# Kernel tuning notes

Hardware: AMD Instinct MI355X
Metric: run time of the kernel (lower is better)

The kernel has to match this reference:

```python
import jax, jax.numpy as jnp
import numpy as np

B, IN, E, H, V, T = 512, 256, 256, 512, 32000, 32


def setup_inputs() -> dict:
    key = jax.random.key(0)
    ks = jax.random.split(key, 8)
    s = 0.05
    return {
        "x": jax.random.normal(ks[0], (B, IN), jnp.float32),
        "agent_w": jax.random.normal(ks[1], (H, IN), jnp.float32) * s,
        "agent_b": jnp.zeros((H,), jnp.float32),
        "sos": jax.random.normal(ks[2], (E,), jnp.float32) * 0.01,
        "emb": jax.random.normal(ks[3], (V, E), jnp.float32) * s,
        "W_ih": jax.random.normal(ks[4], (3 * H, E), jnp.float32) * s,
        "W_hh": jax.random.normal(ks[5], (3 * H, H), jnp.float32) * s,
        "b_ih": jnp.zeros((3 * H,), jnp.float32),
        "b_hh": jnp.zeros((3 * H,), jnp.float32),
        "W_out": jax.random.normal(ks[6], (V, H), jnp.float32) * s,
        "b_out": jnp.zeros((V,), jnp.float32),
        "W_stop": jax.random.normal(ks[7], (1, H), jnp.float32) * s,
        "b_stop": jnp.zeros((1,), jnp.float32),
    }


def _gru_cell(inp, h, W_ih, W_hh, b_ih, b_hh):
    gi = inp @ W_ih.T + b_ih              # [B, 3H]
    gh = h @ W_hh.T + b_hh                # [B, 3H]
    i_r, i_z, i_n = jnp.split(gi, 3, axis=1)
    h_r, h_z, h_n = jnp.split(gh, 3, axis=1)
    r = jax.nn.sigmoid(i_r + h_r)
    z = jax.nn.sigmoid(i_z + h_z)
    n = jnp.tanh(i_n + r * h_n)
    return (1.0 - z) * n + z * h


def reference(x, agent_w, agent_b, sos, emb, W_ih, W_hh, b_ih, b_hh,
              W_out, b_out, W_stop, b_stop):
    h0 = x @ agent_w.T + agent_b                       # agent(x) -> [B, H]
    inp0 = jnp.broadcast_to(sos, (x.shape[0], sos.shape[0]))
    keys = jax.random.split(jax.random.key(42), T)

    def step(carry, k):
        h, inp = carry
        h = _gru_cell(inp, h, W_ih, W_hh, b_ih, b_hh)  # noise_scale=0 -> no noise
        symb_logits = h @ W_out.T + b_out              # [B, V]
        stop_logit = (h @ W_stop.T + b_stop)[:, 0]     # [B]
        logp = jax.nn.log_softmax(symb_logits, axis=1)
        k1, k2 = jax.random.split(k)
        symb = jax.random.categorical(k1, symb_logits, axis=1)          # [B] int
        p_stop = jax.nn.sigmoid(stop_logit)
        stop = jax.random.bernoulli(k2, p_stop).astype(jnp.float32)     # [B]
        symb_lp = jnp.take_along_axis(logp, symb[:, None], axis=1)[:, 0]
        # Bernoulli: log p = s - softplus(s), log(1-p) = -softplus(s)
        sp = jax.nn.softplus(stop_logit)
        stop_lp = stop * stop_logit - sp
        symb_ent = -jnp.sum(jnp.exp(logp) * logp, axis=1)
        stop_ent = sp - stop_logit * p_stop
        inp_next = emb[symb]
        return (h, inp_next), (symb, stop, symb_lp, stop_lp, symb_ent, stop_ent)

    _, ys = jax.lax.scan(step, (h0, inp0), keys)
    symb_seq, stop_seq, symb_lp, stop_lp, symb_ent, stop_ent = ys
    # [T, B] -> [B, T]
    tr = lambda a: a.T
    return (tr(symb_seq), tr(stop_seq).astype(jnp.int32),
            tr(symb_lp), tr(stop_lp), tr(symb_ent), tr(stop_ent))
```

## Files before the change

### kernel.cpp

```cpp
#include <hip/hip_runtime.h>
#include <hip/hip_bf16.h>
#include <stdint.h>

#define JAX_PARTITIONABLE 1

#define Bz 512
#define INz 256
#define Ez 256
#define Hz 512
#define Vz 32000
#define Tz 32
#define BTz (Bz * Tz)
#define TINYF 1.17549435e-38f

typedef float otype;
__device__ __forceinline__ void store_out(otype* out, int idx, float v) {
  out[idx] = v;
}

__device__ __forceinline__ uint32_t rotl32(uint32_t x, int r) {
  return (x << r) | (x >> (32 - r));
}
__device__ __forceinline__ void threefry2x32(uint32_t k0, uint32_t k1,
                                             uint32_t x0, uint32_t x1,
                                             uint32_t& o0, uint32_t& o1) {
  const uint32_t ks2 = k0 ^ k1 ^ 0x1BD11BDAu;
  x0 += k0; x1 += k1;
#define TF_R4(a, b, c, d)                              \
  x0 += x1; x1 = rotl32(x1, a); x1 ^= x0;              \
  x0 += x1; x1 = rotl32(x1, b); x1 ^= x0;              \
  x0 += x1; x1 = rotl32(x1, c); x1 ^= x0;              \
  x0 += x1; x1 = rotl32(x1, d); x1 ^= x0;
  TF_R4(13, 15, 26, 6)  x0 += k1;  x1 += ks2 + 1u;
  TF_R4(17, 29, 16, 24) x0 += ks2; x1 += k0 + 2u;
  TF_R4(13, 15, 26, 6)  x0 += k0;  x1 += k1 + 3u;
  TF_R4(17, 29, 16, 24) x0 += k1;  x1 += ks2 + 4u;
  TF_R4(13, 15, 26, 6)  x0 += ks2; x1 += k0 + 5u;
#undef TF_R4
  o0 = x0; o1 = x1;
}
__device__ __forceinline__ uint32_t rand_bits32(uint32_t ka, uint32_t kb,
                                                uint32_t idx, uint32_t n) {
#if JAX_PARTITIONABLE
  (void)n;
  uint32_t o0, o1;
  threefry2x32(ka, kb, 0u, idx, o0, o1);
  return o0 ^ o1;
#else
  uint32_t half = n >> 1;
  uint32_t o0, o1;
  if (idx < half) { threefry2x32(ka, kb, idx, idx + half, o0, o1); return o0; }
  threefry2x32(ka, kb, idx - half, idx, o0, o1); return o1;
#endif
}
__device__ __forceinline__ float bits_to_f01(uint32_t bits) {
  return __uint_as_float((bits >> 9) | 0x3f800000u) - 1.0f;
}

__global__ void RnnSenderReinforce_36799279792759_kernel(otype* __restrict__ out,
                                                         int n, float v) {
  int i = blockIdx.x * 256 + threadIdx.x;
  if (i < n) out[i] = v;
}

__global__ void keys_kernel(uint32_t* __restrict__ keys) {
  int t = threadIdx.x;
  if (t >= Tz) return;
  uint32_t ka, kb;
#if JAX_PARTITIONABLE
  threefry2x32(0u, 42u, 0u, (uint32_t)t, ka, kb);
#else
  {
    uint32_t j0 = 2u * t, j1 = 2u * t + 1u;
    uint32_t a0, a1, b0, b1;
    if (j0 < Tz) { threefry2x32(0u, 42u, j0, j0 + Tz, a0, a1); ka = a0; }
    else         { threefry2x32(0u, 42u, j0 - Tz, j0, a0, a1); ka = a1; }
    if (j1 < Tz) { threefry2x32(0u, 42u, j1, j1 + Tz, b0, b1); kb = b0; }
    else         { threefry2x32(0u, 42u, j1 - Tz, j1, b0, b1); kb = b1; }
  }
#endif
  uint32_t o0, o1;
#if JAX_PARTITIONABLE
  threefry2x32(ka, kb, 0u, 0u, o0, o1);
  keys[t * 4 + 0] = o0; keys[t * 4 + 1] = o1;
  threefry2x32(ka, kb, 0u, 1u, o0, o1);
  keys[t * 4 + 2] = o0; keys[t * 4 + 3] = o1;
#else
  uint32_t p0, p1, q0, q1;
  threefry2x32(ka, kb, 0u, 2u, p0, p1);
  threefry2x32(ka, kb, 1u, 3u, q0, q1);
  keys[t * 4 + 0] = p0; keys[t * 4 + 1] = q0;
  keys[t * 4 + 2] = p1; keys[t * 4 + 3] = q1;
#endif
}

#define GBM 64
#define GBN 64
#define GBK 32
#define LDSS 68

__device__ __forceinline__ void gemm_bt_body(const float* __restrict__ A,
                                             const float* __restrict__ W,
                                             const float* __restrict__ bias,
                                             float* __restrict__ C,
                                             int M, int N, int K,
                                             int bx, int by,
                                             float* As, float* Bs) {
  const int tid = threadIdx.x;
  const int tx = tid & 15;
  const int ty = tid >> 4;
  const int m0 = by * GBM;
  const int n0 = bx * GBN;
  const int lr = tid >> 3;
  const int lc = (tid & 7) << 2;

  float acc[4][4] = {};
  const float* Ap = A + (size_t)(m0 + lr) * K + lc;
  const float* Wp = W + (size_t)(n0 + lr) * K + lc;
  const size_t rstep = (size_t)32 * K;

  for (int k0 = 0; k0 < K; k0 += GBK) {
    float4 a0 = *(const float4*)(Ap + k0);
    float4 a1 = *(const float4*)(Ap + k0 + rstep);
    float4 b0 = *(const float4*)(Wp + k0);
    float4 b1 = *(const float4*)(Wp + k0 + rstep);
    __syncthreads();
    As[(lc + 0) * LDSS + lr] = a0.x;
    As[(lc + 1) * LDSS + lr] = a0.y;
    As[(lc + 2) * LDSS + lr] = a0.z;
    As[(lc + 3) * LDSS + lr] = a0.w;
    As[(lc + 0) * LDSS + lr + 32] = a1.x;
    As[(lc + 1) * LDSS + lr + 32] = a1.y;
    As[(lc + 2) * LDSS + lr + 32] = a1.z;
    As[(lc + 3) * LDSS + lr + 32] = a1.w;
    Bs[(lc + 0) * LDSS + lr] = b0.x;
    Bs[(lc + 1) * LDSS + lr] = b0.y;
    Bs[(lc + 2) * LDSS + lr] = b0.z;
    Bs[(lc + 3) * LDSS + lr] = b0.w;
    Bs[(lc + 0) * LDSS + lr + 32] = b1.x;
    Bs[(lc + 1) * LDSS + lr + 32] = b1.y;
    Bs[(lc + 2) * LDSS + lr + 32] = b1.z;
    Bs[(lc + 3) * LDSS + lr + 32] = b1.w;
    __syncthreads();
#pragma unroll
    for (int kk = 0; kk < GBK; kk++) {
      float4 af = *(const float4*)&As[kk * LDSS + (ty << 2)];
      float4 bf = *(const float4*)&Bs[kk * LDSS + (tx << 2)];
      float ar[4] = {af.x, af.y, af.z, af.w};
      float br[4] = {bf.x, bf.y, bf.z, bf.w};
#pragma unroll
      for (int i = 0; i < 4; i++)
#pragma unroll
        for (int j = 0; j < 4; j++)
          acc[i][j] = fmaf(ar[i], br[j], acc[i][j]);
    }
  }

  const int nc = n0 + (tx << 2);
  float4 bv;
  bv.x = bias[nc + 0]; bv.y = bias[nc + 1]; bv.z = bias[nc + 2]; bv.w = bias[nc + 3];
#pragma unroll
  for (int i = 0; i < 4; i++) {
    int m = m0 + (ty << 2) + i;
    float4 o;
    o.x = acc[i][0] + bv.x;
    o.y = acc[i][1] + bv.y;
    o.z = acc[i][2] + bv.z;
    o.w = acc[i][3] + bv.w;
    *(float4*)(C + (size_t)m * N + nc) = o;
  }
}

__global__ __launch_bounds__(256) void gemm_bt(const float* __restrict__ A,
                                               const float* __restrict__ W,
                                               const float* __restrict__ bias,
                                               float* __restrict__ C,
                                               int M, int N, int K) {
  __shared__ __align__(16) float As[GBK * LDSS];
  __shared__ __align__(16) float Bs[GBK * LDSS];
  gemm_bt_body(A, W, bias, C, M, N, K, blockIdx.x, blockIdx.y, As, Bs);
}

__global__ __launch_bounds__(256) void gru2_kernel(const float* __restrict__ inp,
                                                   const float* __restrict__ Wih,
                                                   const float* __restrict__ bih,
                                                   float* __restrict__ gi,
                                                   const float* __restrict__ h,
                                                   const float* __restrict__ Whh,
                                                   const float* __restrict__ bhh,
                                                   float* __restrict__ gh) {
  __shared__ __align__(16) float As[GBK * LDSS];
  __shared__ __align__(16) float Bs[GBK * LDSS];
  if (blockIdx.z == 0)
    gemm_bt_body(inp, Wih, bih, gi, Bz, 3 * Hz, Ez, blockIdx.x, blockIdx.y, As, Bs);
  else
    gemm_bt_body(h, Whh, bhh, gh, Bz, 3 * Hz, Hz, blockIdx.x, blockIdx.y, As, Bs);
}

#define QBM 256
#define QBN 128
#define QBK 32
#define QLDA 260
#define QLDB 132

__global__ __launch_bounds__(512, 4) void gemm256_bt(const float* __restrict__ A,
                                                     const float* __restrict__ W,
                                                     const float* __restrict__ bias,
                                                     float* __restrict__ C,
                                                     int M, int N, int K) {
  __shared__ __align__(16) float As[QBK * QLDA];
  __shared__ __align__(16) float Bs[QBK * QLDB];
  const int tid = threadIdx.x;
  const int tx = tid & 15;
  const int ty = tid >> 4;

  const int nP = N / QBN;
  const int G = nP >> 3;
  const int lim = G << 4;
  int b = blockIdx.x;
  int P, mi;
  if (b < lim) {
    int g = b >> 4, r = b & 15;
    mi = r >> 3;
    P = (g << 3) + (r & 7);
  } else {
    int e = b - lim;
    P = (G << 3) + (e & 1);
    mi = e >> 1;
  }
  const int m0 = mi * QBM;
  const int n0 = P * QBN;

  const int ar = tid >> 1;
  const int ak = (tid & 1) << 4;
  const int br = tid >> 2;
  const int bk = (tid & 3) << 2;

  const float* Ap = A + (size_t)(m0 + ar) * K + ak;
  const float* Wp = W + (size_t)(n0 + br) * K + bk;

  float4 a0 = *(const float4*)(Ap);
  float4 a1 = *(const float4*)(Ap + 4);
  float4 a2 = *(const float4*)(Ap + 8);
  float4 a3 = *(const float4*)(Ap + 12);
  float4 b0 = *(const float4*)(Wp);
  float4 b1 = *(const float4*)(Wp + 16);

  float acc[8][8] = {};

  for (int k0 = 0; k0 < K; k0 += QBK) {
    __syncthreads();
    As[(ak + 0) * QLDA + ar] = a0.x;
    As[(ak + 1) * QLDA + ar] = a0.y;
    As[(ak + 2) * QLDA + ar] = a0.z;
    As[(ak + 3) * QLDA + ar] = a0.w;
    As[(ak + 4) * QLDA + ar] = a1.x;
    As[(ak + 5) * QLDA + ar] = a1.y;
    As[(ak + 6) * QLDA + ar] = a1.z;
    As[(ak + 7) * QLDA + ar] = a1.w;
    As[(ak + 8) * QLDA + ar] = a2.x;
    As[(ak + 9) * QLDA + ar] = a2.y;
    As[(ak + 10) * QLDA + ar] = a2.z;
    As[(ak + 11) * QLDA + ar] = a2.w;
    As[(ak + 12) * QLDA + ar] = a3.x;
    As[(ak + 13) * QLDA + ar] = a3.y;
    As[(ak + 14) * QLDA + ar] = a3.z;
    As[(ak + 15) * QLDA + ar] = a3.w;
    Bs[(bk + 0) * QLDB + br] = b0.x;
    Bs[(bk + 1) * QLDB + br] = b0.y;
    Bs[(bk + 2) * QLDB + br] = b0.z;
    Bs[(bk + 3) * QLDB + br] = b0.w;
    Bs[(16 + bk + 0) * QLDB + br] = b1.x;
    Bs[(16 + bk + 1) * QLDB + br] = b1.y;
    Bs[(16 + bk + 2) * QLDB + br] = b1.z;
    Bs[(16 + bk + 3) * QLDB + br] = b1.w;
    __syncthreads();
    if (k0 + QBK < K) {
      a0 = *(const float4*)(Ap + k0 + QBK);
      a1 = *(const float4*)(Ap + k0 + QBK + 4);
      a2 = *(const float4*)(Ap + k0 + QBK + 8);
      a3 = *(const float4*)(Ap + k0 + QBK + 12);
      b0 = *(const float4*)(Wp + k0 + QBK);
      b1 = *(const float4*)(Wp + k0 + QBK + 16);
    }
#pragma unroll 4
    for (int kk = 0; kk < QBK; kk++) {
      float4 xa0 = *(const float4*)&As[kk * QLDA + (ty << 2)];
      float4 xa1 = *(const float4*)&As[kk * QLDA + 128 + (ty << 2)];
      float4 xb0 = *(const float4*)&Bs[kk * QLDB + (tx << 2)];
      float4 xb1 = *(const float4*)&Bs[kk * QLDB + 64 + (tx << 2)];
      float ar8[8] = {xa0.x, xa0.y, xa0.z, xa0.w, xa1.x, xa1.y, xa1.z, xa1.w};
      float br8[8] = {xb0.x, xb0.y, xb0.z, xb0.w, xb1.x, xb1.y, xb1.z, xb1.w};
#pragma unroll
      for (int i = 0; i < 8; i++)
#pragma unroll
        for (int j = 0; j < 8; j++)
          acc[i][j] = fmaf(ar8[i], br8[j], acc[i][j]);
    }
  }

  const int nc0 = n0 + (tx << 2);
  const float4 bv0 = *(const float4*)(bias + nc0);
  const float4 bv1 = *(const float4*)(bias + nc0 + 64);
#pragma unroll
  for (int hf = 0; hf < 2; hf++) {
#pragma unroll
    for (int i = 0; i < 4; i++) {
      const int m = m0 + hf * 128 + (ty << 2) + i;
      float* Cp = C + (size_t)m * N + nc0;
      float4 o;
      o.x = acc[hf * 4 + i][0] + bv0.x;
      o.y = acc[hf * 4 + i][1] + bv0.y;
      o.z = acc[hf * 4 + i][2] + bv0.z;
      o.w = acc[hf * 4 + i][3] + bv0.w;
      *(float4*)Cp = o;
      float4 o2;
      o2.x = acc[hf * 4 + i][4] + bv1.x;
      o2.y = acc[hf * 4 + i][5] + bv1.y;
      o2.z = acc[hf * 4 + i][6] + bv1.z;
      o2.w = acc[hf * 4 + i][7] + bv1.w;
      *(float4*)(Cp + 64) = o2;
    }
  }
}

__global__ __launch_bounds__(512) void gates_stop_kernel(
    const float* __restrict__ gi, const float* __restrict__ gh,
    float* __restrict__ h, const float* __restrict__ W_stop,
    const float* __restrict__ b_stop, const uint32_t* __restrict__ keys,
    int t, otype* __restrict__ out) {
  __shared__ float hrow[Hz];
  const int b = blockIdx.x;
  const int j = threadIdx.x;
  const float* gib = gi + (size_t)b * (3 * Hz);
  const float* ghb = gh + (size_t)b * (3 * Hz);
  float ir = gib[j], iz = gib[j + Hz], in_ = gib[j + 2 * Hz];
  float hr = ghb[j], hz = ghb[j + Hz], hn = ghb[j + 2 * Hz];
  float r = 1.0f / (1.0f + expf(-(ir + hr)));
  float z = 1.0f / (1.0f + expf(-(iz + hz)));
  float n = tanhf(in_ + r * hn);
  float hv = h[(size_t)b * Hz + j];
  float hnew = (1.0f - z) * n + z * hv;
  h[(size_t)b * Hz + j] = hnew;
  hrow[j] = hnew;
  __syncthreads();
  if (j < 64) {
    const int lane = j;
    float s = 0.0f;
    for (int k = lane; k < Hz; k += 64) s = fmaf(hrow[k], W_stop[k], s);
#pragma unroll
    for (int off = 32; off; off >>= 1) s += __shfl_down(s, off, 64);
    if (lane == 0) {
      s += b_stop[0];
      uint32_t bits = rand_bits32(keys[t * 4 + 2], keys[t * 4 + 3], (uint32_t)b, Bz);
      float u = bits_to_f01(bits);
      float p = 1.0f / (1.0f + expf(-s));
      float stop = (u < p) ? 1.0f : 0.0f;
      float sp = fmaxf(s, 0.0f) + log1pf(expf(-fabsf(s)));
      store_out(out, 1 * BTz + b * Tz + t, stop);
      store_out(out, 3 * BTz + b * Tz + t, stop * s - sp);
      store_out(out, 5 * BTz + b * Tz + t, sp - s * p);
    }
  }
}

__global__ __launch_bounds__(1024) void sample_kernel(const float* __restrict__ logits,
                                                      const uint32_t* __restrict__ keys,
                                                      int t, otype* __restrict__ out,
                                                      const float* __restrict__ emb,
                                                      float* __restrict__ inp) {
  __shared__ float sm4[1024], sg4[1024], sgl4[1024];
  __shared__ int sgi4[1024];
  __shared__ float sm[256], sg[256], sgl[256], sz[256], ss[256];
  __shared__ int sgi[256];
  __shared__ int ssymb;
  const int tid4 = threadIdx.x;
  const int tid = tid4 & 255;
  const int sub = tid4 >> 8;
  const int b = blockIdx.x;
  const float* lb = logits + (size_t)b * Vz;
  const uint32_t k1a = keys[t * 4 + 0], k1b = keys[t * 4 + 1];
  const uint32_t base = (uint32_t)b * (uint32_t)Vz;

  float m = -INFINITY, gbest = -INFINITY, glogit = 0.0f;
  int gidx = 0x7FFFFFFF;
  for (int v = tid + (sub << 8); v < Vz; v += 1024) {
    float l = lb[v];
    m = fmaxf(m, l);
    uint32_t bits = rand_bits32(k1a, k1b, base + (uint32_t)v, (uint32_t)Bz * Vz);
    float f = bits_to_f01(bits);
    float u = fmaxf(TINYF, f + TINYF);
    float g = -logf(-logf(u));
    float val = l + g;
    if (val > gbest) { gbest = val; gidx = v; glogit = l; }
  }
  sm4[tid4] = m; sg4[tid4] = gbest; sgi4[tid4] = gidx; sgl4[tid4] = glogit;
  __syncthreads();
  if (tid4 < 256) {
#pragma unroll
    for (int s4 = 1; s4 < 4; s4++) {
      int o = tid4 + (s4 << 8);
      m = fmaxf(m, sm4[o]);
      float go = sg4[o]; int io = sgi4[o];
      if (go > gbest || (go == gbest && io < gidx)) {
        gbest = go; gidx = io; glogit = sgl4[o];
      }
    }
    sm[tid4] = m; sg[tid4] = gbest; sgi[tid4] = gidx; sgl[tid4] = glogit;
  }
  __syncthreads();
  for (int s2 = 128; s2; s2 >>= 1) {
    if (tid4 < s2) {
      sm[tid4] = fmaxf(sm[tid4], sm[tid4 + s2]);
      float go = sg[tid4 + s2]; int io = sgi[tid4 + s2];
      if (go > sg[tid4] || (go == sg[tid4] && io < sgi[tid4])) {
        sg[tid4] = go; sgi[tid4] = io; sgl[tid4] = sgl[tid4 + s2];
      }
    }
    __syncthreads();
  }
  const float M = sm[0];

  if (tid4 < 256) {
    float Z = 0.0f, S1 = 0.0f;
    for (int v = tid4; v < Vz; v += 256) {
      float sft = lb[v] - M;
      float e = expf(sft);
      Z += e;
      S1 = fmaf(e, sft, S1);
    }
    sz[tid4] = Z; ss[tid4] = S1;
  }
  __syncthreads();
  for (int s2 = 128; s2; s2 >>= 1) {
    if (tid4 < s2) { sz[tid4] += sz[tid4 + s2]; ss[tid4] += ss[tid4 + s2]; }
    __syncthreads();
  }
  if (tid4 == 0) {
    float Zt = sz[0], S1t = ss[0];
    float lse = logf(Zt);
    int symb = sgi[0];
    store_out(out, 0 * BTz + b * Tz + t, (float)symb);
    store_out(out, 2 * BTz + b * Tz + t, (sgl[0] - M) - lse);
    store_out(out, 4 * BTz + b * Tz + t, lse - S1t / Zt);
    ssymb = symb;
  }
  __syncthreads();
  if (tid4 < Ez) {
    int s = ssymb;
    s = (s < 0) ? 0 : ((s >= Vz) ? (Vz - 1) : s);
    inp[(size_t)b * Ez + tid4] = emb[(size_t)s * Ez + tid4];
  }
}

__global__ void init_inp_kernel(float* __restrict__ inp, const float* __restrict__ sos) {
  inp[blockIdx.x * Ez + threadIdx.x] = sos[threadIdx.x];
}

extern "C" __attribute__((visibility("default")))
void kernel_launch(void* const* d_in, const int* in_sizes, int n_in,
                   void* d_out, int out_size, void* d_ws, size_t ws_size,
                   hipStream_t stream) {
  const float* x       = (const float*)d_in[0];
  const float* agent_w = (const float*)d_in[1];
  const float* agent_b = (const float*)d_in[2];
  const float* sos     = (const float*)d_in[3];
  const float* emb     = (const float*)d_in[4];
  const float* W_ih    = (const float*)d_in[5];
  const float* W_hh    = (const float*)d_in[6];
  const float* b_ih    = (const float*)d_in[7];
  const float* b_hh    = (const float*)d_in[8];
  const float* W_out   = (const float*)d_in[9];
  const float* b_out   = (const float*)d_in[10];
  const float* W_stop  = (const float*)d_in[11];
  const float* b_stop  = (const float*)d_in[12];
  otype* out = (otype*)d_out;

  float* ws = (float*)d_ws;
  float* h      = ws;
  float* inp    = h + (size_t)Bz * Hz;
  float* gi     = inp + (size_t)Bz * Ez;
  float* gh     = gi + (size_t)Bz * 3 * Hz;
  float* logits = gh + (size_t)Bz * 3 * Hz;
  uint32_t* keys = (uint32_t*)(logits + (size_t)Bz * Vz);

  keys_kernel<<<1, 64, 0, stream>>>(keys);
  init_inp_kernel<<<Bz, Ez, 0, stream>>>(inp, sos);
  gemm_bt<<<dim3(Hz / GBN, Bz / GBM), 256, 0, stream>>>(x, agent_w, agent_b, h,
                                                        Bz, Hz, INz);
  for (int t = 0; t < Tz; t++) {
    gru2_kernel<<<dim3(3 * Hz / GBN, Bz / GBM, 2), 256, 0, stream>>>(
        inp, W_ih, b_ih, gi, h, W_hh, b_hh, gh);
    gates_stop_kernel<<<Bz, 512, 0, stream>>>(gi, gh, h, W_stop, b_stop, keys,
                                              t, out);
    gemm256_bt<<<(Vz / QBN) * (Bz / QBM), 512, 0, stream>>>(h, W_out, b_out,
                                                            logits, Bz, Vz, Hz);
    sample_kernel<<<Bz, 1024, 0, stream>>>(logits, keys, t, out, emb, inp);
  }
}
```

Before: 10.45 ms.

## Split sampling into two kernels, doubling blocks for Gumbel-max scan

The per-row sampling kernel becomes two kernels. The first uses two 1024-thread blocks per batch row, each scanning half the vocabulary for the running max and the Gumbel-max candidate, and writes per-thread partials to workspace reused from the gi/gh buffers. A second 256-thread kernel merges the partials, computes the softmax normalizer and entropy, and gathers the embedding. The goal is more parallelism on the RNG-heavy scan, at the cost of an extra launch per timestep and a partial-results round trip through global memory.

Measured after the change: 11.12 ms. +6.4%, slower.

```diff
diff --git a/kernel.cpp b/kernel.cpp
--- a/kernel.cpp
+++ b/kernel.cpp
@@ -364,27 +364,27 @@
   }
 }
 
-__global__ __launch_bounds__(1024) void sample_kernel(const float* __restrict__ logits,
-                                                      const uint32_t* __restrict__ keys,
-                                                      int t, otype* __restrict__ out,
-                                                      const float* __restrict__ emb,
-                                                      float* __restrict__ inp) {
+__global__ __launch_bounds__(1024) void sample_p1(const float* __restrict__ logits,
+                                                  const uint32_t* __restrict__ keys,
+                                                  int t,
+                                                  float* __restrict__ pm,
+                                                  float* __restrict__ pg,
+                                                  float* __restrict__ pgl,
+                                                  int* __restrict__ pgi) {
   __shared__ float sm4[1024], sg4[1024], sgl4[1024];
   __shared__ int sgi4[1024];
-  __shared__ float sm[256], sg[256], sgl[256], sz[256], ss[256];
-  __shared__ int sgi[256];
-  __shared__ int ssymb;
   const int tid4 = threadIdx.x;
   const int tid = tid4 & 255;
-  const int sub = tid4 >> 8;
-  const int b = blockIdx.x;
+  const int b = blockIdx.x >> 1;
+  const int S = blockIdx.x & 1;
+  const int sub = (S << 2) | (tid4 >> 8);
   const float* lb = logits + (size_t)b * Vz;
   const uint32_t k1a = keys[t * 4 + 0], k1b = keys[t * 4 + 1];
   const uint32_t base = (uint32_t)b * (uint32_t)Vz;
 
   float m = -INFINITY, gbest = -INFINITY, glogit = 0.0f;
   int gidx = 0x7FFFFFFF;
-  for (int v = tid + (sub << 8); v < Vz; v += 1024) {
+  for (int v = tid + (sub << 8); v < Vz; v += 2048) {
     float l = lb[v];
     m = fmaxf(m, l);
     uint32_t bits = rand_bits32(k1a, k1b, base + (uint32_t)v, (uint32_t)Bz * Vz);
@@ -406,37 +406,64 @@
         gbest = go; gidx = io; glogit = sgl4[o];
       }
     }
-    sm[tid4] = m; sg[tid4] = gbest; sgi[tid4] = gidx; sgl[tid4] = glogit;
-  }
+    const int o = ((b << 1) + S) * 256 + tid4;
+    pm[o] = m; pg[o] = gbest; pgl[o] = glogit; pgi[o] = gidx;
+  }
+}
+
+__global__ __launch_bounds__(256) void sample_p2(const float* __restrict__ logits,
+                                                 const float* __restrict__ pm,
+                                                 const float* __restrict__ pg,
+                                                 const float* __restrict__ pgl,
+                                                 const int* __restrict__ pgi,
+                                                 int t, otype* __restrict__ out,
+                                                 const float* __restrict__ emb,
+                                                 float* __restrict__ inp) {
+  __shared__ float sm[256], sg[256], sgl[256], sz[256], ss[256];
+  __shared__ int sgi[256];
+  __shared__ int ssymb;
+  const int tid = threadIdx.x;
+  const int b = blockIdx.x;
+  const float* lb = logits + (size_t)b * Vz;
+
+  const int o0 = (b << 1) * 256 + tid;
+  const int o1 = o0 + 256;
+  float m = fmaxf(pm[o0], pm[o1]);
+  float gbest = pg[o0]; int gidx = pgi[o0]; float glogit = pgl[o0];
+  {
+    float go = pg[o1]; int io = pgi[o1];
+    if (go > gbest || (go == gbest && io < gidx)) {
+      gbest = go; gidx = io; glogit = pgl[o1];
+    }
+  }
+  sm[tid] = m; sg[tid] = gbest; sgi[tid] = gidx; sgl[tid] = glogit;
   __syncthreads();
   for (int s2 = 128; s2; s2 >>= 1) {
-    if (tid4 < s2) {
-      sm[tid4] = fmaxf(sm[tid4], sm[tid4 + s2]);
-      float go = sg[tid4 + s2]; int io = sgi[tid4 + s2];
-      if (go > sg[tid4] || (go == sg[tid4] && io < sgi[tid4])) {
-        sg[tid4] = go; sgi[tid4] = io; sgl[tid4] = sgl[tid4 + s2];
+    if (tid < s2) {
+      sm[tid] = fmaxf(sm[tid], sm[tid + s2]);
+      float go = sg[tid + s2]; int io = sgi[tid + s2];
+      if (go > sg[tid] || (go == sg[tid] && io < sgi[tid])) {
+        sg[tid] = go; sgi[tid] = io; sgl[tid] = sgl[tid + s2];
       }
     }
     __syncthreads();
   }
   const float M = sm[0];
 
-  if (tid4 < 256) {
-    float Z = 0.0f, S1 = 0.0f;
-    for (int v = tid4; v < Vz; v += 256) {
-      float sft = lb[v] - M;
-      float e = expf(sft);
-      Z += e;
-      S1 = fmaf(e, sft, S1);
-    }
-    sz[tid4] = Z; ss[tid4] = S1;
-  }
+  float Z = 0.0f, S1 = 0.0f;
+  for (int v = tid; v < Vz; v += 256) {
+    float sft = lb[v] - M;
+    float e = expf(sft);
+    Z += e;
+    S1 = fmaf(e, sft, S1);
+  }
+  sz[tid] = Z; ss[tid] = S1;
   __syncthreads();
   for (int s2 = 128; s2; s2 >>= 1) {
-    if (tid4 < s2) { sz[tid4] += sz[tid4 + s2]; ss[tid4] += ss[tid4 + s2]; }
+    if (tid < s2) { sz[tid] += sz[tid + s2]; ss[tid] += ss[tid + s2]; }
     __syncthreads();
   }
-  if (tid4 == 0) {
+  if (tid == 0) {
     float Zt = sz[0], S1t = ss[0];
     float lse = logf(Zt);
     int symb = sgi[0];
@@ -446,11 +473,9 @@
     ssymb = symb;
   }
   __syncthreads();
-  if (tid4 < Ez) {
-    int s = ssymb;
-    s = (s < 0) ? 0 : ((s >= Vz) ? (Vz - 1) : s);
-    inp[(size_t)b * Ez + tid4] = emb[(size_t)s * Ez + tid4];
-  }
+  int s = ssymb;
+  s = (s < 0) ? 0 : ((s >= Vz) ? (Vz - 1) : s);
+  inp[(size_t)b * Ez + tid] = emb[(size_t)s * Ez + tid];
 }
 
 __global__ void init_inp_kernel(float* __restrict__ inp, const float* __restrict__ sos) {
@@ -484,6 +509,11 @@
   float* logits = gh + (size_t)Bz * 3 * Hz;
   uint32_t* keys = (uint32_t*)(logits + (size_t)Bz * Vz);
 
+  float* pm = gi;
+  float* pg = gi + 262144;
+  float* pgl = gi + 2 * 262144;
+  int* pgi = (int*)gh;
+
   keys_kernel<<<1, 64, 0, stream>>>(keys);
   init_inp_kernel<<<Bz, Ez, 0, stream>>>(inp, sos);
   gemm_bt<<<dim3(Hz / GBN, Bz / GBM), 256, 0, stream>>>(x, agent_w, agent_b, h,
@@ -495,6 +525,8 @@
                                               t, out);
     gemm256_bt<<<(Vz / QBN) * (Bz / QBM), 512, 0, stream>>>(h, W_out, b_out,
                                                             logits, Bz, Vz, Hz);
-    sample_kernel<<<Bz, 1024, 0, stream>>>(logits, keys, t, out, emb, inp);
-  }
-}
+    sample_p1<<<Bz * 2, 1024, 0, stream>>>(logits, keys, t, pm, pg, pgl, pgi);
+    sample_p2<<<Bz, 256, 0, stream>>>(logits, pm, pg, pgl, pgi, t, out, emb,
+                                      inp);
+  }
+}
```
